# Kernel optimization log

Hardware: AMD Instinct MI355X
Metric: run time of the kernel (lower is better)

Reference implementation:

```python
import jax, jax.numpy as jnp
import numpy as np

B, N, D = 2, 1024, 1024
H = 4
KD = 512          # key_dim = d_model * 0.5
VD = 1024         # value_dim = d_model
DK = KD // H      # 128 head_qk_dim
DV = VD // H      # 256 head_v_dim
LR = 16           # gate_low_rank_dim
GLN = 16.0        # gate_logit_normalizer
EPS = 1e-5


def setup_inputs() -> dict:
    key = jax.random.key(0)
    ks = jax.random.split(key, 10)
    s = 0.02
    return {
        "x": jax.random.normal(ks[0], (B, N, D), jnp.float32),
        "Wq": jax.random.normal(ks[1], (D, KD), jnp.float32) * s,
        "Wk": jax.random.normal(ks[2], (D, KD), jnp.float32) * s,
        "Wv": jax.random.normal(ks[3], (D, VD), jnp.float32) * s,
        "Wg": jax.random.normal(ks[4], (D, VD), jnp.float32) * s,
        "Wgk1": jax.random.normal(ks[5], (D, LR), jnp.float32) * s,
        "Wgk2": jax.random.normal(ks[6], (LR, KD), jnp.float32) * s,
        "bgk2": jax.random.normal(ks[7], (KD,), jnp.float32) * s,
        "Wout": jax.random.normal(ks[8], (VD, D), jnp.float32) * s,
        "rms_w": jnp.ones((DV,), jnp.float32),
    }


def _split_heads(t, h):
    b, n, hd = t.shape
    return t.reshape(b, n, h, hd // h).transpose(0, 2, 1, 3)  # b h n d


def _gla_scan(q, k, v, g):
    # q,k: [b,h,n,dk]; v: [b,h,n,dv]; g: [b,h,n,dk] (log-decay)
    b, h, n, dk = q.shape
    dv = v.shape[-1]
    qT = jnp.moveaxis(q, 2, 0)  # [n,b,h,dk]
    kT = jnp.moveaxis(k, 2, 0)
    vT = jnp.moveaxis(v, 2, 0)
    gT = jnp.moveaxis(g, 2, 0)

    def step(S, inp):
        qt, kt, vt, gt = inp
        # S_t = diag(exp(g_t)) S_{t-1} + k_t v_t^T ; o_t = q_t S_t
        S = S * jnp.exp(gt)[..., None] + kt[..., None] * vt[..., None, :]
        ot = jnp.einsum('bhk,bhkv->bhv', qt, S)
        return S, ot

    S0 = jnp.zeros((b, h, dk, dv), q.dtype)
    _, o = jax.lax.scan(step, S0, (qT, kT, vT, gT))
    return jnp.moveaxis(o, 0, 2)  # [b,h,n,dv]


def reference(x, Wq, Wk, Wv, Wg, Wgk1, Wgk2, bgk2, Wout, rms_w):
    q = _split_heads(x @ Wq, H)
    k = _split_heads(x @ Wk, H)
    v = _split_heads(x @ Wv, H)
    g = jax.nn.log_sigmoid((x @ Wgk1) @ Wgk2 + bgk2) / GLN
    g = jnp.maximum(g, -3.0)  # chunk mode clamp
    g = _split_heads(g, H)
    o = _gla_scan(q, k, v, g)               # [b,h,n,dv]
    o = o.transpose(0, 2, 1, 3)             # [b,n,h,dv]
    # RMSNorm over head_v_dim
    o = o * jax.lax.rsqrt(jnp.mean(o * o, axis=-1, keepdims=True) + EPS) * rms_w
    o = o.reshape(o.shape[0], o.shape[1], VD)
    o = o * jax.nn.silu(x @ Wg)
    return o @ Wout
```

## Files before the change

### kernel.cpp

```cpp
#include <hip/hip_runtime.h>
#include <math.h>


typedef __attribute__((ext_vector_type(4))) float vf4;
typedef __attribute__((ext_vector_type(4))) unsigned int vu4;
typedef __attribute__((ext_vector_type(8))) short short8;

#define DEVI static __device__ __forceinline__
DEVI vf4 vzero() { vf4 x = {0.f, 0.f, 0.f, 0.f}; return x; }

DEVI float bf2f(unsigned int u) {
  union { unsigned int i; float f; } c; c.i = u << 16; return c.f;
}
DEVI unsigned short f2bf(float f) {
  union { float f; unsigned int i; } c; c.f = f;
  unsigned int i = c.i;
  return (unsigned short)((i + 0x7fffu + ((i >> 16) & 1u)) >> 16);
}
DEVI void unpack8(vu4 r, float* f) {
  f[0] = bf2f(r.x & 0xffffu); f[1] = bf2f(r.x >> 16);
  f[2] = bf2f(r.y & 0xffffu); f[3] = bf2f(r.y >> 16);
  f[4] = bf2f(r.z & 0xffffu); f[5] = bf2f(r.z >> 16);
  f[6] = bf2f(r.w & 0xffffu); f[7] = bf2f(r.w >> 16);
}
DEVI vu4 pack8(const float* f) {
  vu4 o;
  o.x = (unsigned int)f2bf(f[0]) | ((unsigned int)f2bf(f[1]) << 16);
  o.y = (unsigned int)f2bf(f[2]) | ((unsigned int)f2bf(f[3]) << 16);
  o.z = (unsigned int)f2bf(f[4]) | ((unsigned int)f2bf(f[5]) << 16);
  o.w = (unsigned int)f2bf(f[6]) | ((unsigned int)f2bf(f[7]) << 16);
  return o;
}

DEVI void gld16(const unsigned short* g, unsigned short* l) {
  __builtin_amdgcn_global_load_lds(
      (const __attribute__((address_space(1))) unsigned int*)g,
      (__attribute__((address_space(3))) unsigned int*)l,
      16, 0, 0);
}

__global__ __launch_bounds__(256)
void prep_k(const float* __restrict__ Wq, const float* __restrict__ Wk,
            const float* __restrict__ Wv, const float* __restrict__ Wg,
            const float* __restrict__ Wo, const float* __restrict__ X,
            unsigned short* __restrict__ wqT, unsigned short* __restrict__ wkT,
            unsigned short* __restrict__ wvT, unsigned short* __restrict__ wgT,
            unsigned short* __restrict__ woT, unsigned short* __restrict__ xb) {
  __shared__ float T[64][65];
  const int ct = blockIdx.x, kt = blockIdx.y;
  const int t = threadIdx.x;
  const int r = t >> 2, s = t & 3;
  if (ct >= 64) {
    const int rt = ct - 64;
    const size_t base = (size_t)(rt * 64 + r) * 1024 + kt * 64 + s * 16;
    float f[16];
    *(vf4*)&f[0]  = *(const vf4*)(X + base);
    *(vf4*)&f[4]  = *(const vf4*)(X + base + 4);
    *(vf4*)&f[8]  = *(const vf4*)(X + base + 8);
    *(vf4*)&f[12] = *(const vf4*)(X + base + 12);
    *(vu4*)(xb + base) = pack8(f);
    *(vu4*)(xb + base + 8) = pack8(f + 8);
    return;
  }
  const float* W; unsigned short* O; int N; int cb;
  if (ct < 8)       { W = Wq; O = wqT; N = 512;  cb = ct; }
  else if (ct < 16) { W = Wk; O = wkT; N = 512;  cb = ct - 8; }
  else if (ct < 32) { W = Wv; O = wvT; N = 1024; cb = ct - 16; }
  else if (ct < 48) { W = Wg; O = wgT; N = 1024; cb = ct - 32; }
  else              { W = Wo; O = woT; N = 1024; cb = ct - 48; }
  const float* src = W + (size_t)(kt * 64 + r) * N + cb * 64 + s * 16;
#pragma unroll
  for (int u = 0; u < 4; ++u) {
    vf4 v4 = *(const vf4*)(src + u * 4);
    T[r][s * 16 + u * 4 + 0] = v4.x;
    T[r][s * 16 + u * 4 + 1] = v4.y;
    T[r][s * 16 + u * 4 + 2] = v4.z;
    T[r][s * 16 + u * 4 + 3] = v4.w;
  }
  __syncthreads();
  unsigned int pk[8];
#pragma unroll
  for (int u = 0; u < 8; ++u) {
    unsigned int lo = f2bf(T[s * 16 + 2 * u][r]);
    unsigned int hi = f2bf(T[s * 16 + 2 * u + 1][r]);
    pk[u] = lo | (hi << 16);
  }
  unsigned short* dst = O + (size_t)(cb * 64 + r) * 1024 + kt * 64 + s * 16;
  *(vu4*)dst = *(vu4*)&pk[0];
  *(vu4*)(dst + 8) = *(vu4*)&pk[4];
}

__global__ __launch_bounds__(256)
void proj_mfma_k(const unsigned short* __restrict__ xb,
                 const unsigned short* __restrict__ wqT, const unsigned short* __restrict__ wkT,
                 const unsigned short* __restrict__ wvT, const unsigned short* __restrict__ wgT,
                 unsigned short* __restrict__ qb, unsigned short* __restrict__ kb,
                 unsigned short* __restrict__ vb, unsigned short* __restrict__ sgb) {
  __shared__ __align__(16) unsigned short As[128 * 64];
  __shared__ __align__(16) unsigned short Bs[128 * 64];
  const int t = threadIdx.x;
  const int m0 = blockIdx.y << 7;
  const int nt = blockIdx.x;
  const unsigned short* WT; int n0; int kind;
  if (nt < 4)       { WT = wqT; n0 = nt << 7;        kind = 0; }
  else if (nt < 8)  { WT = wkT; n0 = (nt - 4) << 7;  kind = 1; }
  else if (nt < 16) { WT = wvT; n0 = (nt - 8) << 7;  kind = 2; }
  else              { WT = wgT; n0 = (nt - 16) << 7; kind = 3; }

  const int w = t >> 6, lane = t & 63;
  const int wm = (w >> 1) << 6, wn = (w & 1) << 6;
  const int qd = lane >> 4, m = lane & 15;
  const int srow = lane >> 3;
  const int scol = ((lane & 7) ^ srow) << 3;

  vf4 acc[4][4];
#pragma unroll
  for (int i = 0; i < 4; ++i)
#pragma unroll
    for (int j = 0; j < 4; ++j) acc[i][j] = vzero();

  for (int k0 = 0; k0 < 1024; k0 += 64) {
    __syncthreads();
#pragma unroll
    for (int cc = 0; cc < 4; ++cc) {
      const int c = (w << 2) + cc;
      const int row = (c << 3) + srow;
      gld16(xb + (size_t)(m0 + row) * 1024 + k0 + scol, (unsigned short*)As + (c << 9));
      gld16(WT + (size_t)(n0 + row) * 1024 + k0 + scol, (unsigned short*)Bs + (c << 9));
    }
    __syncthreads();
#pragma unroll
    for (int ks = 0; ks < 2; ++ks) {
      const int sw = (((ks << 2) + qd) ^ (m & 7)) << 3;
      short8 af[4], bf[4];
#pragma unroll
      for (int i = 0; i < 4; ++i)
        af[i] = *(const short8*)&As[(wm + i * 16 + m) * 64 + sw];
#pragma unroll
      for (int j = 0; j < 4; ++j)
        bf[j] = *(const short8*)&Bs[(wn + j * 16 + m) * 64 + sw];
#pragma unroll
      for (int i = 0; i < 4; ++i)
#pragma unroll
        for (int j = 0; j < 4; ++j)
          acc[i][j] = __builtin_amdgcn_mfma_f32_16x16x32_bf16(af[i], bf[j], acc[i][j], 0, 0, 0);
    }
  }
#pragma unroll
  for (int i = 0; i < 4; ++i) {
#pragma unroll
    for (int j = 0; j < 4; ++j) {
#pragma unroll
      for (int r = 0; r < 4; ++r) {
        const int grow = m0 + wm + i * 16 + qd * 4 + r;
        const int gcol = n0 + wn + j * 16 + m;
        float val = acc[i][j][r];
        if (kind == 0)      qb[(size_t)grow * 512 + gcol] = f2bf(val);
        else if (kind == 1) kb[(size_t)grow * 512 + gcol] = f2bf(val);
        else if (kind == 2) vb[(size_t)grow * 1024 + gcol] = f2bf(val);
        else {
          val = val / (1.f + expf(-val));
          sgb[(size_t)grow * 1024 + gcol] = f2bf(val);
        }
      }
    }
  }
}

__global__ __launch_bounds__(256)
void out_mfma_k(const unsigned short* __restrict__ Ab,
                const unsigned short* __restrict__ woT, float* __restrict__ Y) {
  __shared__ __align__(16) unsigned short As[64 * 64];
  __shared__ __align__(16) unsigned short Bs[128 * 64];
  const int t = threadIdx.x;
  const int m0 = blockIdx.y << 6;
  const int n0 = blockIdx.x << 7;
  const int w = t >> 6, lane = t & 63;
  const int wm = (w >> 1) * 32, wn = (w & 1) * 64;
  const int qd = lane >> 4, m = lane & 15;
  const int srow = lane >> 3;
  const int scol = ((lane & 7) ^ srow) << 3;

  vf4 acc[2][4];
#pragma unroll
  for (int i = 0; i < 2; ++i)
#pragma unroll
    for (int j = 0; j < 4; ++j) acc[i][j] = vzero();

  for (int k0 = 0; k0 < 1024; k0 += 64) {
    __syncthreads();
#pragma unroll
    for (int cc = 0; cc < 2; ++cc) {
      const int c = (w << 1) + cc;
      const int row = (c << 3) + srow;
      gld16(Ab + (size_t)(m0 + row) * 1024 + k0 + scol, (unsigned short*)As + (c << 9));
    }
#pragma unroll
    for (int cc = 0; cc < 4; ++cc) {
      const int c = (w << 2) + cc;
      const int row = (c << 3) + srow;
      gld16(woT + (size_t)(n0 + row) * 1024 + k0 + scol, (unsigned short*)Bs + (c << 9));
    }
    __syncthreads();
#pragma unroll
    for (int ks = 0; ks < 2; ++ks) {
      const int sw = (((ks << 2) + qd) ^ (m & 7)) << 3;
      short8 af[2], bf[4];
#pragma unroll
      for (int i = 0; i < 2; ++i)
        af[i] = *(const short8*)&As[(wm + i * 16 + m) * 64 + sw];
#pragma unroll
      for (int j = 0; j < 4; ++j)
        bf[j] = *(const short8*)&Bs[(wn + j * 16 + m) * 64 + sw];
#pragma unroll
      for (int i = 0; i < 2; ++i)
#pragma unroll
        for (int j = 0; j < 4; ++j)
          acc[i][j] = __builtin_amdgcn_mfma_f32_16x16x32_bf16(af[i], bf[j], acc[i][j], 0, 0, 0);
    }
  }
#pragma unroll
  for (int i = 0; i < 2; ++i)
#pragma unroll
    for (int j = 0; j < 4; ++j)
#pragma unroll
      for (int r = 0; r < 4; ++r) {
        const int grow = m0 + wm + i * 16 + qd * 4 + r;
        const int gcol = n0 + wn + j * 16 + m;
        Y[(size_t)grow * 1024 + gcol] = acc[i][j][r];
      }
}

__global__ __launch_bounds__(64)
void lowrank_k(const float* __restrict__ X, const float* __restrict__ W1,
               float* __restrict__ xl) {
  const int row = blockIdx.x;
  const int t = threadIdx.x;
  float acc[16];
#pragma unroll
  for (int c2 = 0; c2 < 16; ++c2) acc[c2] = 0.f;
  const float* xp = X + (size_t)row * 1024 + t * 16;
  float xv[16];
#pragma unroll
  for (int u = 0; u < 4; ++u)
    *(vf4*)&xv[u * 4] = *(const vf4*)(xp + u * 4);
#pragma unroll
  for (int j = 0; j < 16; ++j) {
    const float* wp = W1 + (size_t)(t * 16 + j) * 16;
    float wv[16];
#pragma unroll
    for (int u = 0; u < 4; ++u)
      *(vf4*)&wv[u * 4] = *(const vf4*)(wp + u * 4);
#pragma unroll
    for (int c2 = 0; c2 < 16; ++c2) acc[c2] = fmaf(xv[j], wv[c2], acc[c2]);
  }
#pragma unroll
  for (int mm = 1; mm < 64; mm <<= 1) {
#pragma unroll
    for (int c2 = 0; c2 < 16; ++c2) acc[c2] += __shfl_xor(acc[c2], mm, 64);
  }
  if (t == 0) {
#pragma unroll
    for (int c2 = 0; c2 < 16; ++c2) xl[(size_t)row * 16 + c2] = acc[c2];
  }
}

__global__ __launch_bounds__(256)
void gate_scan_k(const float* __restrict__ xl, const float* __restrict__ W2,
                 const float* __restrict__ bias,
                 unsigned short* __restrict__ q, unsigned short* __restrict__ k,
                 float* __restrict__ ebtot) {
  const int t = threadIdx.x;
  const int w = t >> 6, lane = t & 63;
  const int wid = blockIdx.x * 4 + w;
  const int kt = wid & 31;
  const int c = (wid >> 5) & 15;
  const int b = wid >> 9;
  const int kbase = kt * 16;
  const size_t rowbase = (size_t)b * 1024 + c * 64;

  const float* xp = xl + (rowbase + lane) * 16;
  float xv[16];
#pragma unroll
  for (int u = 0; u < 4; ++u)
    *(vf4*)&xv[u * 4] = *(const vf4*)(xp + u * 4);

  const size_t a = (rowbase + lane) * 512 + kbase;
  vu4 qr0 = *(const vu4*)(q + a), qr1 = *(const vu4*)(q + a + 8);
  vu4 kr0 = *(const vu4*)(k + a), kr1 = *(const vu4*)(k + a + 8);
  float qf[16], kf[16];
  unpack8(qr0, qf); unpack8(qr1, qf + 8);
  unpack8(kr0, kf); unpack8(kr1, kf + 8);

  float gf[16];
#pragma unroll
  for (int cc = 0; cc < 16; ++cc) {
    const int col = kbase + cc;
    float z = bias[col];
#pragma unroll
    for (int j = 0; j < 16; ++j) z = fmaf(xv[j], W2[j * 512 + col], z);
    float ls = fminf(z, 0.f) - log1pf(expf(-fabsf(z)));
    float g = fmaxf(ls * (1.f / 16.f), -3.f);
#pragma unroll
    for (int d = 1; d < 64; d <<= 1) {
      float up = __shfl_up(g, d, 64);
      if (lane >= d) g += up;
    }
    qf[cc] *= expf(g);
    kf[cc] *= expf(fminf(-g, 80.f));
    gf[cc] = g;
  }
  *(vu4*)(q + a) = pack8(qf);
  *(vu4*)(q + a + 8) = pack8(qf + 8);
  *(vu4*)(k + a) = pack8(kf);
  *(vu4*)(k + a + 8) = pack8(kf + 8);
  if (lane == 63) {
    float* ep = ebtot + ((size_t)b * 16 + c) * 512 + kbase;
#pragma unroll
    for (int cc = 0; cc < 16; ++cc) ep[cc] = expf(gf[cc]);
  }
}

__global__ __launch_bounds__(256)
void intra_kv_k(const unsigned short* __restrict__ q16, const unsigned short* __restrict__ k16,
                const unsigned short* __restrict__ v, float* __restrict__ o,
                unsigned short* __restrict__ ST) {
  __shared__ __align__(16) unsigned short Qs[64 * 136];
  __shared__ __align__(16) unsigned short Ks[64 * 136];
  __shared__ __align__(16) unsigned short Kt[128 * 68];
  __shared__ __align__(16) unsigned short Vt[128 * 68];
  __shared__ __align__(16) unsigned short Asb[64 * 68];
  const int t = threadIdx.x;
  const int vh = blockIdx.x, c = blockIdx.y, bh = blockIdx.z;
  const int b = bh >> 2, h = bh & 3;
  const size_t rowbase = (size_t)b * 1024 + c * 64;

#pragma unroll
  for (int u2 = 0; u2 < 4; ++u2) {
    const int id = t + (u2 << 8);
    const int row = id >> 4, kg = id & 15;
    vu4 rq = *(const vu4*)(q16 + (rowbase + row) * 512 + h * 128 + kg * 8);
    *(vu4*)&Qs[row * 136 + kg * 8] = rq;
    vu4 rk = *(const vu4*)(k16 + (rowbase + row) * 512 + h * 128 + kg * 8);
    *(vu4*)&Ks[row * 136 + kg * 8] = rk;
    const unsigned short* kp = (const unsigned short*)&rk;
#pragma unroll
    for (int u = 0; u < 8; ++u)
      Kt[(kg * 8 + u) * 68 + row] = kp[u];
    vu4 rv = *(const vu4*)(v + (rowbase + row) * 1024 + h * 256 + vh * 128 + kg * 8);
    const unsigned short* vp = (const unsigned short*)&rv;
#pragma unroll
    for (int u = 0; u < 8; ++u)
      Vt[(kg * 8 + u) * 68 + row] = vp[u];
  }
  __syncthreads();

  const int w = t >> 6, lane = t & 63;
  const int qd = lane >> 4, m = lane & 15;

  {
    short8 af[4];
#pragma unroll
    for (int kf = 0; kf < 4; ++kf)
      af[kf] = *(const short8*)&Qs[(w * 16 + m) * 136 + kf * 32 + qd * 8];
    vf4 acc[4];
#pragma unroll
    for (int jt = 0; jt < 4; ++jt) acc[jt] = vzero();
#pragma unroll
    for (int jt = 0; jt < 4; ++jt)
#pragma unroll
      for (int kf = 0; kf < 4; ++kf) {
        short8 bfr = *(const short8*)&Ks[(jt * 16 + m) * 136 + kf * 32 + qd * 8];
        acc[jt] = __builtin_amdgcn_mfma_f32_16x16x32_bf16(af[kf], bfr, acc[jt], 0, 0, 0);
      }
#pragma unroll
    for (int jt = 0; jt < 4; ++jt)
#pragma unroll
      for (int r = 0; r < 4; ++r) {
        const int i = w * 16 + qd * 4 + r;
        const int j = jt * 16 + m;
        Asb[i * 68 + j] = f2bf((j <= i) ? acc[jt][r] : 0.f);
      }
  }
  __syncthreads();

  {
    vf4 acc2[4][2];
#pragma unroll
    for (int mt = 0; mt < 4; ++mt) { acc2[mt][0] = vzero(); acc2[mt][1] = vzero(); }
#pragma unroll
    for (int kf = 0; kf < 2; ++kf) {
      short8 bf0 = *(const short8*)&Vt[(w * 32 + m) * 68 + kf * 32 + qd * 8];
      short8 bf1 = *(const short8*)&Vt[(w * 32 + 16 + m) * 68 + kf * 32 + qd * 8];
#pragma unroll
      for (int mt = 0; mt < 4; ++mt) {
        short8 af = *(const short8*)&Asb[(mt * 16 + m) * 68 + kf * 32 + qd * 8];
        acc2[mt][0] = __builtin_amdgcn_mfma_f32_16x16x32_bf16(af, bf0, acc2[mt][0], 0, 0, 0);
        acc2[mt][1] = __builtin_amdgcn_mfma_f32_16x16x32_bf16(af, bf1, acc2[mt][1], 0, 0, 0);
      }
    }
#pragma unroll
    for (int mt = 0; mt < 4; ++mt)
#pragma unroll
      for (int nt = 0; nt < 2; ++nt)
#pragma unroll
        for (int r = 0; r < 4; ++r) {
          const int i = mt * 16 + qd * 4 + r;
          const int vc = h * 256 + vh * 128 + w * 32 + nt * 16 + m;
          o[(rowbase + i) * 1024 + vc] = acc2[mt][nt][r];
        }
  }

  {
    short8 af3[2][2];
#pragma unroll
    for (int mt = 0; mt < 2; ++mt)
#pragma unroll
      for (int kf = 0; kf < 2; ++kf)
        af3[mt][kf] = *(const short8*)&Vt[(w * 32 + mt * 16 + m) * 68 + kf * 32 + qd * 8];
#pragma unroll
    for (int nt = 0; nt < 8; ++nt) {
      vf4 a0 = vzero(), a1 = vzero();
#pragma unroll
      for (int kf = 0; kf < 2; ++kf) {
        short8 bfr = *(const short8*)&Kt[(nt * 16 + m) * 68 + kf * 32 + qd * 8];
        a0 = __builtin_amdgcn_mfma_f32_16x16x32_bf16(af3[0][kf], bfr, a0, 0, 0, 0);
        a1 = __builtin_amdgcn_mfma_f32_16x16x32_bf16(af3[1][kf], bfr, a1, 0, 0, 0);
      }
      const size_t sbase = (size_t)(bh * 16 + c) * 256 + vh * 128 + w * 32;
#pragma unroll
      for (int r = 0; r < 4; ++r) {
        ST[(sbase + qd * 4 + r) * 128 + nt * 16 + m] = f2bf(a0[r]);
        ST[(sbase + 16 + qd * 4 + r) * 128 + nt * 16 + m] = f2bf(a1[r]);
      }
    }
  }
}

__global__ __launch_bounds__(256)
void state_scan_k(unsigned short* __restrict__ ST, const float* __restrict__ ebtot) {
  const int idx = blockIdx.x * 256 + threadIdx.x;
  const int kg = idx & 15;
  const int vv = (idx >> 4) & 255;
  const int bh = idx >> 12;
  const int b = bh >> 2, h = bh & 3;
  float s[8];
#pragma unroll
  for (int u = 0; u < 8; ++u) s[u] = 0.f;
  for (int c = 0; c < 16; ++c) {
    unsigned short* p = ST + ((size_t)(bh * 16 + c) * 256 + vv) * 128 + kg * 8;
    const float* ep = ebtot + ((size_t)b * 16 + c) * 512 + h * 128 + kg * 8;
    float e[8];
    *(vf4*)&e[0] = *(const vf4*)ep;
    *(vf4*)&e[4] = *(const vf4*)(ep + 4);
    float kv[8];
    unpack8(*(const vu4*)p, kv);
    *(vu4*)p = pack8(s);
#pragma unroll
    for (int u = 0; u < 8; ++u) s[u] = (s[u] + kv[u]) * e[u];
  }
}

__global__ __launch_bounds__(256)
void o_inter_k(const unsigned short* __restrict__ q16, const unsigned short* __restrict__ ST,
               float* __restrict__ o) {
  __shared__ __align__(16) unsigned short Qs[64 * 136];
  __shared__ __align__(16) unsigned short Ss[128 * 136];
  const int t = threadIdx.x;
  const int vt = blockIdx.x, c = blockIdx.y, bh = blockIdx.z;
  const int b = bh >> 2, h = bh & 3;
  const size_t rowbase = (size_t)b * 1024 + c * 64;

#pragma unroll
  for (int u2 = 0; u2 < 4; ++u2) {
    const int id = t + (u2 << 8);
    const int row = id >> 4, kg = id & 15;
    *(vu4*)&Qs[row * 136 + kg * 8] =
        *(const vu4*)(q16 + (rowbase + row) * 512 + h * 128 + kg * 8);
  }
#pragma unroll
  for (int u2 = 0; u2 < 8; ++u2) {
    const int id = t + (u2 << 8);
    const int vrow = id >> 4, kg = id & 15;
    *(vu4*)&Ss[vrow * 136 + kg * 8] =
        *(const vu4*)(ST + ((size_t)(bh * 16 + c) * 256 + vt * 128 + vrow) * 128 + kg * 8);
  }
  __syncthreads();

  const int w = t >> 6, lane = t & 63;
  const int qd = lane >> 4, m = lane & 15;
  short8 af[4];
#pragma unroll
  for (int kf = 0; kf < 4; ++kf)
    af[kf] = *(const short8*)&Qs[(w * 16 + m) * 136 + kf * 32 + qd * 8];
#pragma unroll
  for (int nt = 0; nt < 8; ++nt) {
    vf4 acc = vzero();
#pragma unroll
    for (int kf = 0; kf < 4; ++kf) {
      short8 bfr = *(const short8*)&Ss[(nt * 16 + m) * 136 + kf * 32 + qd * 8];
      acc = __builtin_amdgcn_mfma_f32_16x16x32_bf16(af[kf], bfr, acc, 0, 0, 0);
    }
    float* base = o + (rowbase + w * 16 + qd * 4) * 1024 + h * 256 + vt * 128 + nt * 16 + m;
#pragma unroll
    for (int r = 0; r < 4; ++r)
      base[(size_t)r * 1024] += acc[r];
  }
}

__global__ __launch_bounds__(256)
void norm_gate_k(const float* __restrict__ o, const float* __restrict__ rmsw,
                 const unsigned short* __restrict__ sg,
                 unsigned short* __restrict__ ob) {
  __shared__ float red[4];
  const int grp = blockIdx.x;
  const int row = grp >> 2, h = grp & 3;
  const int t = threadIdx.x;
  const size_t idx = (size_t)row * 1024 + h * 256 + t;
  const float val = o[idx];
  float ss = val * val;
#pragma unroll
  for (int mm = 1; mm < 64; mm <<= 1) ss += __shfl_xor(ss, mm, 64);
  if ((t & 63) == 0) red[t >> 6] = ss;
  __syncthreads();
  const float tot = red[0] + red[1] + red[2] + red[3];
  const float scale = rsqrtf(tot * (1.f / 256.f) + 1e-5f);
  ob[idx] = f2bf(val * scale * rmsw[t] * bf2f((unsigned int)sg[idx]));
}

extern "C" void kernel_launch(void* const* d_in, const int* in_sizes, int n_in,
                              void* d_out, int out_size, void* d_ws, size_t ws_size,
                              hipStream_t stream) {
  const float* x    = (const float*)d_in[0];
  const float* Wq   = (const float*)d_in[1];
  const float* Wk   = (const float*)d_in[2];
  const float* Wv   = (const float*)d_in[3];
  const float* Wg   = (const float*)d_in[4];
  const float* Wgk1 = (const float*)d_in[5];
  const float* Wgk2 = (const float*)d_in[6];
  const float* bgk2 = (const float*)d_in[7];
  const float* Wout = (const float*)d_in[8];
  const float* rmsw = (const float*)d_in[9];

  const size_t MB = 1u << 20;
  char* w = (char*)d_ws;
  unsigned short* qb16   = (unsigned short*)(w);
  unsigned short* kb16   = (unsigned short*)(w + 2 * MB);
  unsigned short* vbuf   = (unsigned short*)(w + 4 * MB);
  unsigned short* sgbuf  = (unsigned short*)(w + 8 * MB);
  float*          obuf   = (float*)(w + 12 * MB);
  char*           sreg   = w + 20 * MB;
  unsigned short* xb     = (unsigned short*)sreg;
  unsigned short* STbuf  = (unsigned short*)sreg;
  unsigned short* obuf_b = (unsigned short*)sreg;
  float*          xlbuf  = (float*)(w + 28 * MB);
  float*          ebbuf  = (float*)(w + 28 * MB + 131072);
  unsigned short* wqT    = (unsigned short*)(w + 29 * MB);
  unsigned short* wkT    = (unsigned short*)(w + 30 * MB);
  unsigned short* wvT    = (unsigned short*)(w + 31 * MB);
  unsigned short* wgT    = (unsigned short*)(w + 33 * MB);
  unsigned short* woT    = (unsigned short*)(w + 35 * MB);

  prep_k<<<dim3(96, 16), 256, 0, stream>>>(Wq, Wk, Wv, Wg, Wout, x,
                                           wqT, wkT, wvT, wgT, woT, xb);
  lowrank_k<<<2048, 64, 0, stream>>>(x, Wgk1, xlbuf);
  proj_mfma_k<<<dim3(24, 16), 256, 0, stream>>>(xb, wqT, wkT, wvT, wgT, qb16, kb16, vbuf, sgbuf);
  gate_scan_k<<<256, 256, 0, stream>>>(xlbuf, Wgk2, bgk2, qb16, kb16, ebbuf);
  intra_kv_k<<<dim3(2, 16, 8), 256, 0, stream>>>(qb16, kb16, vbuf, obuf, STbuf);
  state_scan_k<<<128, 256, 0, stream>>>(STbuf, ebbuf);
  o_inter_k<<<dim3(2, 16, 8), 256, 0, stream>>>(qb16, STbuf, obuf);
  norm_gate_k<<<8192, 256, 0, stream>>>(obuf, rmsw, sgbuf, obuf_b);
  out_mfma_k<<<dim3(8, 32), 256, 0, stream>>>(obuf_b, woT, (float*)d_out);
}
```

Measured before the change: 194.2 us.

## Fuse scan stages and output stages into persistent kernels with grid barriers

Merges prep and lowrank into a single launch, and merges gate scan, intra-chunk KV, state scan and inter-chunk output into one 256-block kernel that separates phases with atomic grid barriers. Norm-gate and the output GEMM are likewise fused behind a grid barrier, with the norm vectorised so each wave handles several rows. The aim is to cut launch overhead and inter-kernel gaps across nine launches reduced to four. It relies on all 256 blocks being co-resident for the spin barriers, and the barrier counters are reset by the first kernel.

```diff
diff --git a/kernel.cpp b/kernel.cpp
--- a/kernel.cpp
+++ b/kernel.cpp
@@ -5,6 +5,7 @@
 typedef __attribute__((ext_vector_type(4))) float vf4;
 typedef __attribute__((ext_vector_type(4))) unsigned int vu4;
 typedef __attribute__((ext_vector_type(8))) short short8;
+typedef __attribute__((ext_vector_type(4))) unsigned short us4;
 
 #define DEVI static __device__ __forceinline__
 DEVI vf4 vzero() { vf4 x = {0.f, 0.f, 0.f, 0.f}; return x; }
@@ -39,16 +40,66 @@
       16, 0, 0);
 }
 
+DEVI void gridbar(unsigned* c, unsigned tgt) {
+  __syncthreads();
+  if (threadIdx.x == 0) {
+    __threadfence();
+    __hip_atomic_fetch_add(c, 1u, __ATOMIC_ACQ_REL, __HIP_MEMORY_SCOPE_AGENT);
+    while (__hip_atomic_load(c, __ATOMIC_ACQUIRE, __HIP_MEMORY_SCOPE_AGENT) < tgt)
+      __builtin_amdgcn_s_sleep(1);
+    __threadfence();
+  }
+  __syncthreads();
+}
+
 __global__ __launch_bounds__(256)
-void prep_k(const float* __restrict__ Wq, const float* __restrict__ Wk,
-            const float* __restrict__ Wv, const float* __restrict__ Wg,
-            const float* __restrict__ Wo, const float* __restrict__ X,
-            unsigned short* __restrict__ wqT, unsigned short* __restrict__ wkT,
-            unsigned short* __restrict__ wvT, unsigned short* __restrict__ wgT,
-            unsigned short* __restrict__ woT, unsigned short* __restrict__ xb) {
+void prep_lowrank_k(const float* __restrict__ Wq, const float* __restrict__ Wk,
+                    const float* __restrict__ Wv, const float* __restrict__ Wg,
+                    const float* __restrict__ Wo, const float* __restrict__ X,
+                    const float* __restrict__ Wgk1,
+                    unsigned short* __restrict__ wqT, unsigned short* __restrict__ wkT,
+                    unsigned short* __restrict__ wvT, unsigned short* __restrict__ wgT,
+                    unsigned short* __restrict__ woT, unsigned short* __restrict__ xb,
+                    float* __restrict__ xl, unsigned* __restrict__ bar) {
   __shared__ float T[64][65];
-  const int ct = blockIdx.x, kt = blockIdx.y;
+  const int bid = blockIdx.x;
   const int t = threadIdx.x;
+  if (bid == 0 && t < 8) bar[t] = 0;
+
+  if (bid >= 1536) {
+    const int w = t >> 6, lane = t & 63;
+    const int row = (bid - 1536) * 4 + w;
+    float acc[16];
+#pragma unroll
+    for (int c2 = 0; c2 < 16; ++c2) acc[c2] = 0.f;
+    const float* xp = X + (size_t)row * 1024 + lane * 16;
+    float xv[16];
+#pragma unroll
+    for (int u = 0; u < 4; ++u)
+      *(vf4*)&xv[u * 4] = *(const vf4*)(xp + u * 4);
+#pragma unroll
+    for (int j = 0; j < 16; ++j) {
+      const float* wp = Wgk1 + (size_t)(lane * 16 + j) * 16;
+      float wv[16];
+#pragma unroll
+      for (int u = 0; u < 4; ++u)
+        *(vf4*)&wv[u * 4] = *(const vf4*)(wp + u * 4);
+#pragma unroll
+      for (int c2 = 0; c2 < 16; ++c2) acc[c2] = fmaf(xv[j], wv[c2], acc[c2]);
+    }
+#pragma unroll
+    for (int mm = 1; mm < 64; mm <<= 1) {
+#pragma unroll
+      for (int c2 = 0; c2 < 16; ++c2) acc[c2] += __shfl_xor(acc[c2], mm, 64);
+    }
+    if (lane == 0) {
+#pragma unroll
+      for (int c2 = 0; c2 < 16; ++c2) xl[(size_t)row * 16 + c2] = acc[c2];
+    }
+    return;
+  }
+
+  const int ct = bid % 96, kt = bid / 96;
   const int r = t >> 2, s = t & 3;
   if (ct >= 64) {
     const int rt = ct - 64;
@@ -168,14 +219,268 @@
 }
 
 __global__ __launch_bounds__(256)
-void out_mfma_k(const unsigned short* __restrict__ Ab,
-                const unsigned short* __restrict__ woT, float* __restrict__ Y) {
+void fused_scan_k(const float* __restrict__ xl, const float* __restrict__ W2,
+                  const float* __restrict__ bias,
+                  unsigned short* __restrict__ q16, unsigned short* __restrict__ k16,
+                  float* __restrict__ ebtot, const unsigned short* __restrict__ v,
+                  float* __restrict__ o, unsigned short* __restrict__ ST,
+                  unsigned* __restrict__ bar) {
+  __shared__ __align__(16) unsigned short L[39168];
+  unsigned short* Qs  = L;
+  unsigned short* Ks  = L + 8704;
+  unsigned short* Kt  = L + 17408;
+  unsigned short* Vt  = L + 26112;
+  unsigned short* Asb = L + 34816;
+  unsigned short* Ss  = L + 8704;
+
+  const int t = threadIdx.x;
+  const int bid = blockIdx.x;
+  const int w = t >> 6, lane = t & 63;
+  const int qd = lane >> 4, m = lane & 15;
+
+  {
+    const int wid = bid * 4 + w;
+    const int kt = wid & 31;
+    const int c = (wid >> 5) & 15;
+    const int b = wid >> 9;
+    const int kbase = kt * 16;
+    const size_t rowbase = (size_t)b * 1024 + c * 64;
+
+    const float* xp = xl + (rowbase + lane) * 16;
+    float xv[16];
+#pragma unroll
+    for (int u = 0; u < 4; ++u)
+      *(vf4*)&xv[u * 4] = *(const vf4*)(xp + u * 4);
+
+    const size_t a = (rowbase + lane) * 512 + kbase;
+    vu4 qr0 = *(const vu4*)(q16 + a), qr1 = *(const vu4*)(q16 + a + 8);
+    vu4 kr0 = *(const vu4*)(k16 + a), kr1 = *(const vu4*)(k16 + a + 8);
+    float qf[16], kf[16];
+    unpack8(qr0, qf); unpack8(qr1, qf + 8);
+    unpack8(kr0, kf); unpack8(kr1, kf + 8);
+
+    float gf[16];
+#pragma unroll
+    for (int cc = 0; cc < 16; ++cc) {
+      const int col = kbase + cc;
+      float z = bias[col];
+#pragma unroll
+      for (int j = 0; j < 16; ++j) z = fmaf(xv[j], W2[j * 512 + col], z);
+      float ls = fminf(z, 0.f) - log1pf(expf(-fabsf(z)));
+      float g = fmaxf(ls * (1.f / 16.f), -3.f);
+#pragma unroll
+      for (int d = 1; d < 64; d <<= 1) {
+        float up = __shfl_up(g, d, 64);
+        if (lane >= d) g += up;
+      }
+      qf[cc] *= expf(g);
+      kf[cc] *= expf(fminf(-g, 80.f));
+      gf[cc] = g;
+    }
+    *(vu4*)(q16 + a) = pack8(qf);
+    *(vu4*)(q16 + a + 8) = pack8(qf + 8);
+    *(vu4*)(k16 + a) = pack8(kf);
+    *(vu4*)(k16 + a + 8) = pack8(kf + 8);
+    if (lane == 63) {
+      float* ep = ebtot + ((size_t)b * 16 + c) * 512 + kbase;
+#pragma unroll
+      for (int cc = 0; cc < 16; ++cc) ep[cc] = expf(gf[cc]);
+    }
+  }
+  gridbar(bar + 0, 256);
+
+  const int vh = bid & 1, c = (bid >> 1) & 15, bh = bid >> 5;
+  const int b = bh >> 2, h = bh & 3;
+  const size_t rowbase = (size_t)b * 1024 + c * 64;
+  {
+#pragma unroll
+    for (int u2 = 0; u2 < 4; ++u2) {
+      const int id = t + (u2 << 8);
+      const int row = id >> 4, kg = id & 15;
+      vu4 rq = *(const vu4*)(q16 + (rowbase + row) * 512 + h * 128 + kg * 8);
+      *(vu4*)&Qs[row * 136 + kg * 8] = rq;
+      vu4 rk = *(const vu4*)(k16 + (rowbase + row) * 512 + h * 128 + kg * 8);
+      *(vu4*)&Ks[row * 136 + kg * 8] = rk;
+      const unsigned short* kp = (const unsigned short*)&rk;
+#pragma unroll
+      for (int u = 0; u < 8; ++u)
+        Kt[(kg * 8 + u) * 68 + row] = kp[u];
+      vu4 rv = *(const vu4*)(v + (rowbase + row) * 1024 + h * 256 + vh * 128 + kg * 8);
+      const unsigned short* vp = (const unsigned short*)&rv;
+#pragma unroll
+      for (int u = 0; u < 8; ++u)
+        Vt[(kg * 8 + u) * 68 + row] = vp[u];
+    }
+    __syncthreads();
+
+    {
+      short8 af[4];
+#pragma unroll
+      for (int kf = 0; kf < 4; ++kf)
+        af[kf] = *(const short8*)&Qs[(w * 16 + m) * 136 + kf * 32 + qd * 8];
+      vf4 acc[4];
+#pragma unroll
+      for (int jt = 0; jt < 4; ++jt) acc[jt] = vzero();
+#pragma unroll
+      for (int jt = 0; jt < 4; ++jt)
+#pragma unroll
+        for (int kf = 0; kf < 4; ++kf) {
+          short8 bfr = *(const short8*)&Ks[(jt * 16 + m) * 136 + kf * 32 + qd * 8];
+          acc[jt] = __builtin_amdgcn_mfma_f32_16x16x32_bf16(af[kf], bfr, acc[jt], 0, 0, 0);
+        }
+#pragma unroll
+      for (int jt = 0; jt < 4; ++jt)
+#pragma unroll
+        for (int r = 0; r < 4; ++r) {
+          const int i = w * 16 + qd * 4 + r;
+          const int j = jt * 16 + m;
+          Asb[i * 68 + j] = f2bf((j <= i) ? acc[jt][r] : 0.f);
+        }
+    }
+    __syncthreads();
+
+    {
+      vf4 acc2[4][2];
+#pragma unroll
+      for (int mt = 0; mt < 4; ++mt) { acc2[mt][0] = vzero(); acc2[mt][1] = vzero(); }
+#pragma unroll
+      for (int kf = 0; kf < 2; ++kf) {
+        short8 bf0 = *(const short8*)&Vt[(w * 32 + m) * 68 + kf * 32 + qd * 8];
+        short8 bf1 = *(const short8*)&Vt[(w * 32 + 16 + m) * 68 + kf * 32 + qd * 8];
+#pragma unroll
+        for (int mt = 0; mt < 4; ++mt) {
+          short8 af = *(const short8*)&Asb[(mt * 16 + m) * 68 + kf * 32 + qd * 8];
+          acc2[mt][0] = __builtin_amdgcn_mfma_f32_16x16x32_bf16(af, bf0, acc2[mt][0], 0, 0, 0);
+          acc2[mt][1] = __builtin_amdgcn_mfma_f32_16x16x32_bf16(af, bf1, acc2[mt][1], 0, 0, 0);
+        }
+      }
+#pragma unroll
+      for (int mt = 0; mt < 4; ++mt)
+#pragma unroll
+        for (int nt = 0; nt < 2; ++nt)
+#pragma unroll
+          for (int r = 0; r < 4; ++r) {
+            const int i = mt * 16 + qd * 4 + r;
+            const int vc = h * 256 + vh * 128 + w * 32 + nt * 16 + m;
+            o[(rowbase + i) * 1024 + vc] = acc2[mt][nt][r];
+          }
+    }
+
+    {
+      short8 af3[2][2];
+#pragma unroll
+      for (int mt = 0; mt < 2; ++mt)
+#pragma unroll
+        for (int kf = 0; kf < 2; ++kf)
+          af3[mt][kf] = *(const short8*)&Vt[(w * 32 + mt * 16 + m) * 68 + kf * 32 + qd * 8];
+#pragma unroll
+      for (int nt = 0; nt < 8; ++nt) {
+        vf4 a0 = vzero(), a1 = vzero();
+#pragma unroll
+        for (int kf = 0; kf < 2; ++kf) {
+          short8 bfr = *(const short8*)&Kt[(nt * 16 + m) * 68 + kf * 32 + qd * 8];
+          a0 = __builtin_amdgcn_mfma_f32_16x16x32_bf16(af3[0][kf], bfr, a0, 0, 0, 0);
+          a1 = __builtin_amdgcn_mfma_f32_16x16x32_bf16(af3[1][kf], bfr, a1, 0, 0, 0);
+        }
+        const size_t sbase = (size_t)(bh * 16 + c) * 256 + vh * 128 + w * 32;
+#pragma unroll
+        for (int r = 0; r < 4; ++r) {
+          ST[(sbase + qd * 4 + r) * 128 + nt * 16 + m] = f2bf(a0[r]);
+          ST[(sbase + 16 + qd * 4 + r) * 128 + nt * 16 + m] = f2bf(a1[r]);
+        }
+      }
+    }
+  }
+  gridbar(bar + 1, 256);
+
+  if (bid < 128) {
+    const int idx = bid * 256 + t;
+    const int kg = idx & 15;
+    const int vv = (idx >> 4) & 255;
+    const int sbh = idx >> 12;
+    const int sb = sbh >> 2, sh = sbh & 3;
+    float s[8];
+#pragma unroll
+    for (int u = 0; u < 8; ++u) s[u] = 0.f;
+    for (int sc = 0; sc < 16; ++sc) {
+      unsigned short* p = ST + ((size_t)(sbh * 16 + sc) * 256 + vv) * 128 + kg * 8;
+      const float* ep = ebtot + ((size_t)sb * 16 + sc) * 512 + sh * 128 + kg * 8;
+      float e[8];
+      *(vf4*)&e[0] = *(const vf4*)ep;
+      *(vf4*)&e[4] = *(const vf4*)(ep + 4);
+      float kv[8];
+      unpack8(*(const vu4*)p, kv);
+      *(vu4*)p = pack8(s);
+#pragma unroll
+      for (int u = 0; u < 8; ++u) s[u] = (s[u] + kv[u]) * e[u];
+    }
+  }
+  gridbar(bar + 2, 256);
+
+  {
+#pragma unroll
+    for (int u2 = 0; u2 < 8; ++u2) {
+      const int id = t + (u2 << 8);
+      const int vrow = id >> 4, kg = id & 15;
+      *(vu4*)&Ss[vrow * 136 + kg * 8] =
+          *(const vu4*)(ST + ((size_t)(bh * 16 + c) * 256 + vh * 128 + vrow) * 128 + kg * 8);
+    }
+    __syncthreads();
+
+    short8 af[4];
+#pragma unroll
+    for (int kf = 0; kf < 4; ++kf)
+      af[kf] = *(const short8*)&Qs[(w * 16 + m) * 136 + kf * 32 + qd * 8];
+#pragma unroll
+    for (int nt = 0; nt < 8; ++nt) {
+      vf4 acc = vzero();
+#pragma unroll
+      for (int kf = 0; kf < 4; ++kf) {
+        short8 bfr = *(const short8*)&Ss[(nt * 16 + m) * 136 + kf * 32 + qd * 8];
+        acc = __builtin_amdgcn_mfma_f32_16x16x32_bf16(af[kf], bfr, acc, 0, 0, 0);
+      }
+      float* base = o + (rowbase + w * 16 + qd * 4) * 1024 + h * 256 + vh * 128 + nt * 16 + m;
+#pragma unroll
+      for (int r = 0; r < 4; ++r)
+        base[(size_t)r * 1024] += acc[r];
+    }
+  }
+}
+
+__global__ __launch_bounds__(256)
+void fused_out_k(const float* __restrict__ o, const float* __restrict__ rmsw,
+                 const unsigned short* __restrict__ sg, unsigned short* __restrict__ ob,
+                 const unsigned short* __restrict__ woT, float* __restrict__ Y,
+                 unsigned* __restrict__ bar) {
   __shared__ __align__(16) unsigned short As[64 * 64];
   __shared__ __align__(16) unsigned short Bs[128 * 64];
   const int t = threadIdx.x;
-  const int m0 = blockIdx.y << 6;
-  const int n0 = blockIdx.x << 7;
+  const int bid = blockIdx.x;
   const int w = t >> 6, lane = t & 63;
+
+#pragma unroll
+  for (int g = 0; g < 8; ++g) {
+    const int grp = (bid * 4 + w) * 8 + g;
+    const int row = grp >> 2, h = grp & 3;
+    const size_t base = (size_t)row * 1024 + h * 256 + lane * 4;
+    vf4 val = *(const vf4*)(o + base);
+    float ss = val.x * val.x + val.y * val.y + val.z * val.z + val.w * val.w;
+#pragma unroll
+    for (int mm = 1; mm < 64; mm <<= 1) ss += __shfl_xor(ss, mm, 64);
+    const float scale = rsqrtf(ss * (1.f / 256.f) + 1e-5f);
+    us4 sgv = *(const us4*)(sg + base);
+    vf4 rw = *(const vf4*)(rmsw + lane * 4);
+    us4 outv;
+    outv.x = f2bf(val.x * scale * rw.x * bf2f((unsigned int)sgv.x));
+    outv.y = f2bf(val.y * scale * rw.y * bf2f((unsigned int)sgv.y));
+    outv.z = f2bf(val.z * scale * rw.z * bf2f((unsigned int)sgv.z));
+    outv.w = f2bf(val.w * scale * rw.w * bf2f((unsigned int)sgv.w));
+    *(us4*)(ob + base) = outv;
+  }
+  gridbar(bar + 3, 256);
+
+  const int m0 = (bid >> 3) << 6;
+  const int n0 = (bid & 7) << 7;
   const int wm = (w >> 1) * 32, wn = (w & 1) * 64;
   const int qd = lane >> 4, m = lane & 15;
   const int srow = lane >> 3;
@@ -193,7 +498,7 @@
     for (int cc = 0; cc < 2; ++cc) {
       const int c = (w << 1) + cc;
       const int row = (c << 3) + srow;
-      gld16(Ab + (size_t)(m0 + row) * 1024 + k0 + scol, (unsigned short*)As + (c << 9));
+      gld16(ob + (size_t)(m0 + row) * 1024 + k0 + scol, (unsigned short*)As + (c << 9));
     }
 #pragma unroll
     for (int cc = 0; cc < 4; ++cc) {
@@ -229,303 +534,6 @@
         const int gcol = n0 + wn + j * 16 + m;
         Y[(size_t)grow * 1024 + gcol] = acc[i][j][r];
       }
-}
-
-__global__ __launch_bounds__(64)
-void lowrank_k(const float* __restrict__ X, const float* __restrict__ W1,
-               float* __restrict__ xl) {
-  const int row = blockIdx.x;
-  const int t = threadIdx.x;
-  float acc[16];
-#pragma unroll
-  for (int c2 = 0; c2 < 16; ++c2) acc[c2] = 0.f;
-  const float* xp = X + (size_t)row * 1024 + t * 16;
-  float xv[16];
-#pragma unroll
-  for (int u = 0; u < 4; ++u)
-    *(vf4*)&xv[u * 4] = *(const vf4*)(xp + u * 4);
-#pragma unroll
-  for (int j = 0; j < 16; ++j) {
-    const float* wp = W1 + (size_t)(t * 16 + j) * 16;
-    float wv[16];
-#pragma unroll
-    for (int u = 0; u < 4; ++u)
-      *(vf4*)&wv[u * 4] = *(const vf4*)(wp + u * 4);
-#pragma unroll
-    for (int c2 = 0; c2 < 16; ++c2) acc[c2] = fmaf(xv[j], wv[c2], acc[c2]);
-  }
-#pragma unroll
-  for (int mm = 1; mm < 64; mm <<= 1) {
-#pragma unroll
-    for (int c2 = 0; c2 < 16; ++c2) acc[c2] += __shfl_xor(acc[c2], mm, 64);
-  }
-  if (t == 0) {
-#pragma unroll
-    for (int c2 = 0; c2 < 16; ++c2) xl[(size_t)row * 16 + c2] = acc[c2];
-  }
-}
-
-__global__ __launch_bounds__(256)
-void gate_scan_k(const float* __restrict__ xl, const float* __restrict__ W2,
-                 const float* __restrict__ bias,
-                 unsigned short* __restrict__ q, unsigned short* __restrict__ k,
-                 float* __restrict__ ebtot) {
-  const int t = threadIdx.x;
-  const int w = t >> 6, lane = t & 63;
-  const int wid = blockIdx.x * 4 + w;
-  const int kt = wid & 31;
-  const int c = (wid >> 5) & 15;
-  const int b = wid >> 9;
-  const int kbase = kt * 16;
-  const size_t rowbase = (size_t)b * 1024 + c * 64;
-
-  const float* xp = xl + (rowbase + lane) * 16;
-  float xv[16];
-#pragma unroll
-  for (int u = 0; u < 4; ++u)
-    *(vf4*)&xv[u * 4] = *(const vf4*)(xp + u * 4);
-
-  const size_t a = (rowbase + lane) * 512 + kbase;
-  vu4 qr0 = *(const vu4*)(q + a), qr1 = *(const vu4*)(q + a + 8);
-  vu4 kr0 = *(const vu4*)(k + a), kr1 = *(const vu4*)(k + a + 8);
-  float qf[16], kf[16];
-  unpack8(qr0, qf); unpack8(qr1, qf + 8);
-  unpack8(kr0, kf); unpack8(kr1, kf + 8);
-
-  float gf[16];
-#pragma unroll
-  for (int cc = 0; cc < 16; ++cc) {
-    const int col = kbase + cc;
-    float z = bias[col];
-#pragma unroll
-    for (int j = 0; j < 16; ++j) z = fmaf(xv[j], W2[j * 512 + col], z);
-    float ls = fminf(z, 0.f) - log1pf(expf(-fabsf(z)));
-    float g = fmaxf(ls * (1.f / 16.f), -3.f);
-#pragma unroll
-    for (int d = 1; d < 64; d <<= 1) {
-      float up = __shfl_up(g, d, 64);
-      if (lane >= d) g += up;
-    }
-    qf[cc] *= expf(g);
-    kf[cc] *= expf(fminf(-g, 80.f));
-    gf[cc] = g;
-  }
-  *(vu4*)(q + a) = pack8(qf);
-  *(vu4*)(q + a + 8) = pack8(qf + 8);
-  *(vu4*)(k + a) = pack8(kf);
-  *(vu4*)(k + a + 8) = pack8(kf + 8);
-  if (lane == 63) {
-    float* ep = ebtot + ((size_t)b * 16 + c) * 512 + kbase;
-#pragma unroll
-    for (int cc = 0; cc < 16; ++cc) ep[cc] = expf(gf[cc]);
-  }
-}
-
-__global__ __launch_bounds__(256)
-void intra_kv_k(const unsigned short* __restrict__ q16, const unsigned short* __restrict__ k16,
-                const unsigned short* __restrict__ v, float* __restrict__ o,
-                unsigned short* __restrict__ ST) {
-  __shared__ __align__(16) unsigned short Qs[64 * 136];
-  __shared__ __align__(16) unsigned short Ks[64 * 136];
-  __shared__ __align__(16) unsigned short Kt[128 * 68];
-  __shared__ __align__(16) unsigned short Vt[128 * 68];
-  __shared__ __align__(16) unsigned short Asb[64 * 68];
-  const int t = threadIdx.x;
-  const int vh = blockIdx.x, c = blockIdx.y, bh = blockIdx.z;
-  const int b = bh >> 2, h = bh & 3;
-  const size_t rowbase = (size_t)b * 1024 + c * 64;
-
-#pragma unroll
-  for (int u2 = 0; u2 < 4; ++u2) {
-    const int id = t + (u2 << 8);
-    const int row = id >> 4, kg = id & 15;
-    vu4 rq = *(const vu4*)(q16 + (rowbase + row) * 512 + h * 128 + kg * 8);
-    *(vu4*)&Qs[row * 136 + kg * 8] = rq;
-    vu4 rk = *(const vu4*)(k16 + (rowbase + row) * 512 + h * 128 + kg * 8);
-    *(vu4*)&Ks[row * 136 + kg * 8] = rk;
-    const unsigned short* kp = (const unsigned short*)&rk;
-#pragma unroll
-    for (int u = 0; u < 8; ++u)
-      Kt[(kg * 8 + u) * 68 + row] = kp[u];
-    vu4 rv = *(const vu4*)(v + (rowbase + row) * 1024 + h * 256 + vh * 128 + kg * 8);
-    const unsigned short* vp = (const unsigned short*)&rv;
-#pragma unroll
-    for (int u = 0; u < 8; ++u)
-      Vt[(kg * 8 + u) * 68 + row] = vp[u];
-  }
-  __syncthreads();
-
-  const int w = t >> 6, lane = t & 63;
-  const int qd = lane >> 4, m = lane & 15;
-
-  {
-    short8 af[4];
-#pragma unroll
-    for (int kf = 0; kf < 4; ++kf)
-      af[kf] = *(const short8*)&Qs[(w * 16 + m) * 136 + kf * 32 + qd * 8];
-    vf4 acc[4];
-#pragma unroll
-    for (int jt = 0; jt < 4; ++jt) acc[jt] = vzero();
-#pragma unroll
-    for (int jt = 0; jt < 4; ++jt)
-#pragma unroll
-      for (int kf = 0; kf < 4; ++kf) {
-        short8 bfr = *(const short8*)&Ks[(jt * 16 + m) * 136 + kf * 32 + qd * 8];
-        acc[jt] = __builtin_amdgcn_mfma_f32_16x16x32_bf16(af[kf], bfr, acc[jt], 0, 0, 0);
-      }
-#pragma unroll
-    for (int jt = 0; jt < 4; ++jt)
-#pragma unroll
-      for (int r = 0; r < 4; ++r) {
-        const int i = w * 16 + qd * 4 + r;
-        const int j = jt * 16 + m;
-        Asb[i * 68 + j] = f2bf((j <= i) ? acc[jt][r] : 0.f);
-      }
-  }
-  __syncthreads();
-
-  {
-    vf4 acc2[4][2];
-#pragma unroll
-    for (int mt = 0; mt < 4; ++mt) { acc2[mt][0] = vzero(); acc2[mt][1] = vzero(); }
-#pragma unroll
-    for (int kf = 0; kf < 2; ++kf) {
-      short8 bf0 = *(const short8*)&Vt[(w * 32 + m) * 68 + kf * 32 + qd * 8];
-      short8 bf1 = *(const short8*)&Vt[(w * 32 + 16 + m) * 68 + kf * 32 + qd * 8];
-#pragma unroll
-      for (int mt = 0; mt < 4; ++mt) {
-        short8 af = *(const short8*)&Asb[(mt * 16 + m) * 68 + kf * 32 + qd * 8];
-        acc2[mt][0] = __builtin_amdgcn_mfma_f32_16x16x32_bf16(af, bf0, acc2[mt][0], 0, 0, 0);
-        acc2[mt][1] = __builtin_amdgcn_mfma_f32_16x16x32_bf16(af, bf1, acc2[mt][1], 0, 0, 0);
-      }
-    }
-#pragma unroll
-    for (int mt = 0; mt < 4; ++mt)
-#pragma unroll
-      for (int nt = 0; nt < 2; ++nt)
-#pragma unroll
-        for (int r = 0; r < 4; ++r) {
-          const int i = mt * 16 + qd * 4 + r;
-          const int vc = h * 256 + vh * 128 + w * 32 + nt * 16 + m;
-          o[(rowbase + i) * 1024 + vc] = acc2[mt][nt][r];
-        }
-  }
-
-  {
-    short8 af3[2][2];
-#pragma unroll
-    for (int mt = 0; mt < 2; ++mt)
-#pragma unroll
-      for (int kf = 0; kf < 2; ++kf)
-        af3[mt][kf] = *(const short8*)&Vt[(w * 32 + mt * 16 + m) * 68 + kf * 32 + qd * 8];
-#pragma unroll
-    for (int nt = 0; nt < 8; ++nt) {
-      vf4 a0 = vzero(), a1 = vzero();
-#pragma unroll
-      for (int kf = 0; kf < 2; ++kf) {
-        short8 bfr = *(const short8*)&Kt[(nt * 16 + m) * 68 + kf * 32 + qd * 8];
-        a0 = __builtin_amdgcn_mfma_f32_16x16x32_bf16(af3[0][kf], bfr, a0, 0, 0, 0);
-        a1 = __builtin_amdgcn_mfma_f32_16x16x32_bf16(af3[1][kf], bfr, a1, 0, 0, 0);
-      }
-      const size_t sbase = (size_t)(bh * 16 + c) * 256 + vh * 128 + w * 32;
-#pragma unroll
-      for (int r = 0; r < 4; ++r) {
-        ST[(sbase + qd * 4 + r) * 128 + nt * 16 + m] = f2bf(a0[r]);
-        ST[(sbase + 16 + qd * 4 + r) * 128 + nt * 16 + m] = f2bf(a1[r]);
-      }
-    }
-  }
-}
-
-__global__ __launch_bounds__(256)
-void state_scan_k(unsigned short* __restrict__ ST, const float* __restrict__ ebtot) {
-  const int idx = blockIdx.x * 256 + threadIdx.x;
-  const int kg = idx & 15;
-  const int vv = (idx >> 4) & 255;
-  const int bh = idx >> 12;
-  const int b = bh >> 2, h = bh & 3;
-  float s[8];
-#pragma unroll
-  for (int u = 0; u < 8; ++u) s[u] = 0.f;
-  for (int c = 0; c < 16; ++c) {
-    unsigned short* p = ST + ((size_t)(bh * 16 + c) * 256 + vv) * 128 + kg * 8;
-    const float* ep = ebtot + ((size_t)b * 16 + c) * 512 + h * 128 + kg * 8;
-    float e[8];
-    *(vf4*)&e[0] = *(const vf4*)ep;
-    *(vf4*)&e[4] = *(const vf4*)(ep + 4);
-    float kv[8];
-    unpack8(*(const vu4*)p, kv);
-    *(vu4*)p = pack8(s);
-#pragma unroll
-    for (int u = 0; u < 8; ++u) s[u] = (s[u] + kv[u]) * e[u];
-  }
-}
-
-__global__ __launch_bounds__(256)
-void o_inter_k(const unsigned short* __restrict__ q16, const unsigned short* __restrict__ ST,
-               float* __restrict__ o) {
-  __shared__ __align__(16) unsigned short Qs[64 * 136];
-  __shared__ __align__(16) unsigned short Ss[128 * 136];
-  const int t = threadIdx.x;
-  const int vt = blockIdx.x, c = blockIdx.y, bh = blockIdx.z;
-  const int b = bh >> 2, h = bh & 3;
-  const size_t rowbase = (size_t)b * 1024 + c * 64;
-
-#pragma unroll
-  for (int u2 = 0; u2 < 4; ++u2) {
-    const int id = t + (u2 << 8);
-    const int row = id >> 4, kg = id & 15;
-    *(vu4*)&Qs[row * 136 + kg * 8] =
-        *(const vu4*)(q16 + (rowbase + row) * 512 + h * 128 + kg * 8);
-  }
-#pragma unroll
-  for (int u2 = 0; u2 < 8; ++u2) {
-    const int id = t + (u2 << 8);
-    const int vrow = id >> 4, kg = id & 15;
-    *(vu4*)&Ss[vrow * 136 + kg * 8] =
-        *(const vu4*)(ST + ((size_t)(bh * 16 + c) * 256 + vt * 128 + vrow) * 128 + kg * 8);
-  }
-  __syncthreads();
-
-  const int w = t >> 6, lane = t & 63;
-  const int qd = lane >> 4, m = lane & 15;
-  short8 af[4];
-#pragma unroll
-  for (int kf = 0; kf < 4; ++kf)
-    af[kf] = *(const short8*)&Qs[(w * 16 + m) * 136 + kf * 32 + qd * 8];
-#pragma unroll
-  for (int nt = 0; nt < 8; ++nt) {
-    vf4 acc = vzero();
-#pragma unroll
-    for (int kf = 0; kf < 4; ++kf) {
-      short8 bfr = *(const short8*)&Ss[(nt * 16 + m) * 136 + kf * 32 + qd * 8];
-      acc = __builtin_amdgcn_mfma_f32_16x16x32_bf16(af[kf], bfr, acc, 0, 0, 0);
-    }
-    float* base = o + (rowbase + w * 16 + qd * 4) * 1024 + h * 256 + vt * 128 + nt * 16 + m;
-#pragma unroll
-    for (int r = 0; r < 4; ++r)
-      base[(size_t)r * 1024] += acc[r];
-  }
-}
-
-__global__ __launch_bounds__(256)
-void norm_gate_k(const float* __restrict__ o, const float* __restrict__ rmsw,
-                 const unsigned short* __restrict__ sg,
-                 unsigned short* __restrict__ ob) {
-  __shared__ float red[4];
-  const int grp = blockIdx.x;
-  const int row = grp >> 2, h = grp & 3;
-  const int t = threadIdx.x;
-  const size_t idx = (size_t)row * 1024 + h * 256 + t;
-  const float val = o[idx];
-  float ss = val * val;
-#pragma unroll
-  for (int mm = 1; mm < 64; mm <<= 1) ss += __shfl_xor(ss, mm, 64);
-  if ((t & 63) == 0) red[t >> 6] = ss;
-  __syncthreads();
-  const float tot = red[0] + red[1] + red[2] + red[3];
-  const float scale = rsqrtf(tot * (1.f / 256.f) + 1e-5f);
-  ob[idx] = f2bf(val * scale * rmsw[t] * bf2f((unsigned int)sg[idx]));
 }
 
 extern "C" void kernel_launch(void* const* d_in, const int* in_sizes, int n_in,
@@ -560,15 +568,12 @@
   unsigned short* wvT    = (unsigned short*)(w + 31 * MB);
   unsigned short* wgT    = (unsigned short*)(w + 33 * MB);
   unsigned short* woT    = (unsigned short*)(w + 35 * MB);
-
-  prep_k<<<dim3(96, 16), 256, 0, stream>>>(Wq, Wk, Wv, Wg, Wout, x,
-                                           wqT, wkT, wvT, wgT, woT, xb);
-  lowrank_k<<<2048, 64, 0, stream>>>(x, Wgk1, xlbuf);
+  unsigned*       bar    = (unsigned*)(w + 37 * MB);
+
+  prep_lowrank_k<<<2048, 256, 0, stream>>>(Wq, Wk, Wv, Wg, Wout, x, Wgk1,
+                                           wqT, wkT, wvT, wgT, woT, xb, xlbuf, bar);
   proj_mfma_k<<<dim3(24, 16), 256, 0, stream>>>(xb, wqT, wkT, wvT, wgT, qb16, kb16, vbuf, sgbuf);
-  gate_scan_k<<<256, 256, 0, stream>>>(xlbuf, Wgk2, bgk2, qb16, kb16, ebbuf);
-  intra_kv_k<<<dim3(2, 16, 8), 256, 0, stream>>>(qb16, kb16, vbuf, obuf, STbuf);
-  state_scan_k<<<128, 256, 0, stream>>>(STbuf, ebbuf);
-  o_inter_k<<<dim3(2, 16, 8), 256, 0, stream>>>(qb16, STbuf, obuf);
-  norm_gate_k<<<8192, 256, 0, stream>>>(obuf, rmsw, sgbuf, obuf_b);
-  out_mfma_k<<<dim3(8, 32), 256, 0, stream>>>(obuf_b, woT, (float*)d_out);
-}
+  fused_scan_k<<<256, 256, 0, stream>>>(xlbuf, Wgk2, bgk2, qb16, kb16, ebbuf, vbuf,
+                                        obuf, STbuf, bar);
+  fused_out_k<<<256, 256, 0, stream>>>(obuf, rmsw, sgbuf, obuf_b, woT, (float*)d_out, bar);
+}
```

New measurement: 325.4 us. 1.68x slower.
